# Kernel tuning notes

Hardware: AMD Instinct MI355X
Metric: run time of the kernel (lower is better)

The kernel has to match this reference:

```python
import jax, jax.numpy as jnp
import numpy as np

B, N, D, S = 4, 8, 64, 8192  # batch, heads, dim_head, seq_len


def setup_inputs() -> dict:
    key = jax.random.key(0)
    kq, kk, kv = jax.random.split(key, 3)
    q = jax.random.normal(kq, (B, N, D, S), dtype=jnp.float32)
    k = jax.random.normal(kk, (B, N, D, S), dtype=jnp.float32)
    v = jax.random.normal(kv, (B, N, D, S), dtype=jnp.float32)
    return {"q": q, "k": k, "v": v}


def reference(q, k, v):
    # q, k, v: [b, n, d, s] = [batch, heads, dim_head, seq]
    scale = q.shape[-2] ** -0.5  # dim_head^-0.5
    qs = jax.nn.softmax(q, axis=-2) * scale   # softmax over feature dim
    ks = jax.nn.softmax(k, axis=-1)           # softmax over seq dim
    # kv context: [b, n, d, d] -- avoids the O(s^2) score matrix
    context = jnp.einsum('bnis,bnjs->bnij', ks, v)
    # out: [b, n, d, s]
    return jnp.einsum('bnij,bnis->bnjs', context, qs)
```

## Files before the change

### kernel.cpp

```cpp
#include <hip/hip_runtime.h>
#include <math.h>


typedef _Float16 half8 __attribute__((ext_vector_type(8)));
typedef float floatx4 __attribute__((ext_vector_type(4)));
typedef float floatx16 __attribute__((ext_vector_type(16)));

constexpr int BHEADS = 32;
constexpr int DH     = 64;
constexpr int SEQ    = 8192;
constexpr int NCHUNK = 32;
constexpr float QSCALE = 0.125f;

__device__ __forceinline__ void gload_lds16(const float* g, float* l)
{
    __builtin_amdgcn_global_load_lds(
        (const __attribute__((address_space(1))) void*)g,
        (__attribute__((address_space(3))) void*)l, 16, 0, 0);
}

__global__ __launch_bounds__(256)
void ctx_partial_kernel(const float* __restrict__ K, const float* __restrict__ V,
                        float* __restrict__ partial, float* __restrict__ Zp)
{
    const int head  = blockIdx.y;
    const int chunk = blockIdx.x;
    const int t     = threadIdx.x;
    const int lane  = t & 63;
    const int w     = t >> 6;
    const int ln    = lane & 15;
    const int q8    = lane >> 4;

    const int s0 = chunk * 256;
    const float* kh = K + (size_t)head * DH * SEQ;
    const float* vh = V + (size_t)head * DH * SEQ;

    __shared__ __align__(16) float kbuf[2][64 * 32];
    __shared__ __align__(16) float vbuf[2][64 * 32];

    const int rl = 16 * w + (lane >> 3);
    const int sg = (lane & 7) ^ (rl & 7);
    const float* kg0 = kh + (size_t)rl * SEQ + s0 + sg * 4;
    const float* kg1 = kg0 + (size_t)8 * SEQ;
    const float* vg0 = vh + (size_t)rl * SEQ + s0 + sg * 4;
    const float* vg1 = vg0 + (size_t)8 * SEQ;

#define STAGE(pb, off)                                          \
    do {                                                        \
        gload_lds16(kg0 + (off), &kbuf[pb][(16 * w) * 32]);     \
        gload_lds16(kg1 + (off), &kbuf[pb][(16 * w + 8) * 32]); \
        gload_lds16(vg0 + (off), &vbuf[pb][(16 * w) * 32]);     \
        gload_lds16(vg1 + (off), &vbuf[pb][(16 * w + 8) * 32]); \
    } while (0)

    STAGE(0, 0);
    __syncthreads();

    floatx4 acc[4];
    #pragma unroll
    for (int jt = 0; jt < 4; ++jt) acc[jt] = (floatx4){0.f, 0.f, 0.f, 0.f};
    float zacc = 0.f;

    const int rA = 16 * w + ln;

    #pragma unroll
    for (int step = 0; step < 8; ++step) {
        const int p = step & 1;
        if (step < 7) STAGE(p ^ 1, (step + 1) * 32);
        float e[8];
        #pragma unroll
        for (int eo = 0; eo < 2; ++eo) {
            const int sl = ((q8 * 2 + eo) ^ (rA & 7)) * 4;
            const float4 kv = *(const float4*)(&kbuf[p][rA * 32 + sl]);
            e[eo * 4 + 0] = __expf(kv.x);
            e[eo * 4 + 1] = __expf(kv.y);
            e[eo * 4 + 2] = __expf(kv.z);
            e[eo * 4 + 3] = __expf(kv.w);
        }
        zacc += e[0]+e[1]+e[2]+e[3]+e[4]+e[5]+e[6]+e[7];
        half8 ah;
        #pragma unroll
        for (int x = 0; x < 8; ++x) ah[x] = (_Float16)e[x];
        #pragma unroll
        for (int jt = 0; jt < 4; ++jt) {
            const int rB = 16 * jt + ln;
            half8 bh;
            #pragma unroll
            for (int eo = 0; eo < 2; ++eo) {
                const int sl = ((q8 * 2 + eo) ^ (rB & 7)) * 4;
                const float4 vv = *(const float4*)(&vbuf[p][rB * 32 + sl]);
                bh[eo * 4 + 0] = (_Float16)vv.x;
                bh[eo * 4 + 1] = (_Float16)vv.y;
                bh[eo * 4 + 2] = (_Float16)vv.z;
                bh[eo * 4 + 3] = (_Float16)vv.w;
            }
            acc[jt] = __builtin_amdgcn_mfma_f32_16x16x32_f16(ah, bh, acc[jt], 0, 0, 0);
        }
        if (step < 7) __syncthreads();
    }
#undef STAGE

    float* ph = partial + (size_t)(head * NCHUNK + chunk) * DH * DH;
    #pragma unroll
    for (int jt = 0; jt < 4; ++jt) {
        #pragma unroll
        for (int rr = 0; rr < 4; ++rr) {
            const int i = 16 * w + q8 * 4 + rr;
            const int j = 16 * jt + ln;
            ph[i * DH + j] = acc[jt][rr];
        }
    }

    zacc += __shfl_xor(zacc, 16);
    zacc += __shfl_xor(zacc, 32);
    if (lane < 16)
        Zp[(head * NCHUNK + chunk) * DH + 16 * w + ln] = zacc;
}

__global__ __launch_bounds__(256)
void reduce_kernel(const float* __restrict__ partial, const float* __restrict__ Zp,
                   _Float16* __restrict__ czT)
{
    const int h  = blockIdx.x >> 4;
    const int ig = blockIdx.x & 15;
    const int t  = threadIdx.x;
    const int il = t >> 6;
    const int j  = t & 63;
    const int i  = 4 * ig + il;

    const float* ph = partial + (size_t)h * NCHUNK * DH * DH + i * DH + j;
    float sum = 0.f;
    #pragma unroll
    for (int c = 0; c < NCHUNK; ++c)
        sum += ph[(size_t)c * DH * DH];

    float z = 0.f;
    #pragma unroll
    for (int c = 0; c < NCHUNK; ++c)
        z += Zp[(h * NCHUNK + c) * DH + i];

    czT[(size_t)h * DH * DH + j * DH + i] = (_Float16)(sum / z);
}

__global__ __launch_bounds__(256)
void out_kernel(const float* __restrict__ Q, const _Float16* __restrict__ czT,
                float* __restrict__ out)
{
    const int head = blockIdx.y;
    const int sb   = blockIdx.x;
    const int t    = threadIdx.x;
    const int lane = t & 63;
    const int w    = t >> 6;
    const int l31  = lane & 31;
    const int lh   = lane >> 5;
    const int jw   = 32 * (w & 1);
    const int sw   = 32 * (w >> 1);

    __shared__ __align__(16) float    qf[64 * 68];
    __shared__ __align__(16) _Float16 eqT[64 * 64];
    __shared__ __align__(16) float    wred[64 * 4];

    const float* qh = Q + (size_t)head * DH * SEQ;
    const int r0 = t >> 4;
    const int sc = 4 * (t & 15);
    const int s0 = sb * 128;

    float4 pq[4];
    #pragma unroll
    for (int p = 0; p < 4; ++p)
        pq[p] = *(const float4*)(qh + (size_t)(r0 + 16 * p) * SEQ + s0 + sc);

    const _Float16* ch = czT + (size_t)head * DH * DH;
    half8 afr[4];
    #pragma unroll
    for (int st = 0; st < 4; ++st)
        afr[st] = *(const half8*)(ch + (jw + l31) * DH + st * 16 + lh * 8);

    for (int r = 0; r < 2; ++r) {
        #pragma unroll
        for (int p = 0; p < 4; ++p)
            *(float4*)(qf + (r0 + 16 * p) * 68 + sc) = pq[p];
        if (r < 1) {
            #pragma unroll
            for (int p = 0; p < 4; ++p)
                pq[p] = *(const float4*)(qh + (size_t)(r0 + 16 * p) * SEQ
                                         + s0 + 64 + sc);
        }
        __syncthreads();
        {
            const int s  = t & 63;
            const int cg = t >> 6;
            float wsum = 0.f;
            #pragma unroll
            for (int h2 = 0; h2 < 2; ++h2) {
                const int cc = cg + 4 * h2;
                half8 p8;
                #pragma unroll
                for (int jj = 0; jj < 8; ++jj) {
                    const float e = __expf(qf[(8 * cc + jj) * 68 + s]);
                    wsum += e;
                    p8[jj] = (_Float16)e;
                }
                *(half8*)(eqT + s * 64 + ((cc ^ (s & 7)) * 8)) = p8;
            }
            wred[s * 4 + cg] = wsum;
        }
        __syncthreads();
        const float4 wv = *(const float4*)(wred + (sw + l31) * 4);
        const float rw = QSCALE / (wv.x + wv.y + wv.z + wv.w);
        floatx16 acc = {};
        #pragma unroll
        for (int st = 0; st < 4; ++st) {
            const int s2 = sw + l31;
            const int cc = 2 * st + lh;
            const half8 b = *(const half8*)(eqT + s2 * 64 + ((cc ^ (s2 & 7)) * 8));
            acc = __builtin_amdgcn_mfma_f32_32x32x16_f16(afr[st], b, acc, 0, 0, 0);
        }
        float* oh = out + (size_t)head * DH * SEQ + s0 + r * 64;
        #pragma unroll
        for (int rg = 0; rg < 16; ++rg) {
            const int j = jw + (rg & 3) + 8 * (rg >> 2) + 4 * lh;
            oh[(size_t)j * SEQ + sw + l31] = acc[rg] * rw;
        }
    }
}

extern "C" void kernel_launch(void* const* d_in, const int* in_sizes, int n_in,
                              void* d_out, int out_size, void* d_ws, size_t ws_size,
                              hipStream_t stream)
{
    const float* q = (const float*)d_in[0];
    const float* k = (const float*)d_in[1];
    const float* v = (const float*)d_in[2];
    float* out = (float*)d_out;

    float*    partial = (float*)d_ws;
    float*    Zp      = partial + BHEADS * NCHUNK * DH * DH;
    _Float16* czT     = (_Float16*)(Zp + BHEADS * NCHUNK * DH);

    ctx_partial_kernel<<<dim3(NCHUNK, BHEADS), 256, 0, stream>>>(k, v, partial, Zp);
    reduce_kernel<<<BHEADS * 16, 256, 0, stream>>>(partial, Zp, czT);
    out_kernel<<<dim3(64, BHEADS), 256, 0, stream>>>(q, czT, out);
}
```

Measured before the change: 243.7 us.

## Load Q directly into MFMA B-fragments in out_kernel, dropping LDS staging

The output kernel no longer stages Q through shared memory with a transpose and two barriers. Each lane now reads its Q column values straight from global memory, exponentiates them, and packs them into the MFMA operand. The per-column softmax sum is completed with a cross-lane shuffle. The grid doubles so each block handles 64 sequence positions with one MFMA tile per wave. This removes LDS traffic and synchronization, but the global loads become 32-lane coalesced scalar reads (128B segments) instead of float4 loads, and duplicate Q reads across the two j-halves double the global read volume for Q.

```diff
diff --git a/kernel.cpp b/kernel.cpp
--- a/kernel.cpp
+++ b/kernel.cpp
@@ -154,21 +154,9 @@
     const int l31  = lane & 31;
     const int lh   = lane >> 5;
     const int jw   = 32 * (w & 1);
-    const int sw   = 32 * (w >> 1);
-
-    __shared__ __align__(16) float    qf[64 * 68];
-    __shared__ __align__(16) _Float16 eqT[64 * 64];
-    __shared__ __align__(16) float    wred[64 * 4];
-
-    const float* qh = Q + (size_t)head * DH * SEQ;
-    const int r0 = t >> 4;
-    const int sc = 4 * (t & 15);
-    const int s0 = sb * 128;
-
-    float4 pq[4];
-    #pragma unroll
-    for (int p = 0; p < 4; ++p)
-        pq[p] = *(const float4*)(qh + (size_t)(r0 + 16 * p) * SEQ + s0 + sc);
+    const int s0   = sb * 64 + 32 * (w >> 1);
+
+    const float* qh = Q + (size_t)head * DH * SEQ + s0 + l31;
 
     const _Float16* ch = czT + (size_t)head * DH * DH;
     half8 afr[4];
@@ -176,52 +164,32 @@
     for (int st = 0; st < 4; ++st)
         afr[st] = *(const half8*)(ch + (jw + l31) * DH + st * 16 + lh * 8);
 
-    for (int r = 0; r < 2; ++r) {
-        #pragma unroll
-        for (int p = 0; p < 4; ++p)
-            *(float4*)(qf + (r0 + 16 * p) * 68 + sc) = pq[p];
-        if (r < 1) {
-            #pragma unroll
-            for (int p = 0; p < 4; ++p)
-                pq[p] = *(const float4*)(qh + (size_t)(r0 + 16 * p) * SEQ
-                                         + s0 + 64 + sc);
-        }
-        __syncthreads();
-        {
-            const int s  = t & 63;
-            const int cg = t >> 6;
-            float wsum = 0.f;
-            #pragma unroll
-            for (int h2 = 0; h2 < 2; ++h2) {
-                const int cc = cg + 4 * h2;
-                half8 p8;
-                #pragma unroll
-                for (int jj = 0; jj < 8; ++jj) {
-                    const float e = __expf(qf[(8 * cc + jj) * 68 + s]);
-                    wsum += e;
-                    p8[jj] = (_Float16)e;
-                }
-                *(half8*)(eqT + s * 64 + ((cc ^ (s & 7)) * 8)) = p8;
-            }
-            wred[s * 4 + cg] = wsum;
-        }
-        __syncthreads();
-        const float4 wv = *(const float4*)(wred + (sw + l31) * 4);
-        const float rw = QSCALE / (wv.x + wv.y + wv.z + wv.w);
-        floatx16 acc = {};
-        #pragma unroll
-        for (int st = 0; st < 4; ++st) {
-            const int s2 = sw + l31;
-            const int cc = 2 * st + lh;
-            const half8 b = *(const half8*)(eqT + s2 * 64 + ((cc ^ (s2 & 7)) * 8));
-            acc = __builtin_amdgcn_mfma_f32_32x32x16_f16(afr[st], b, acc, 0, 0, 0);
-        }
-        float* oh = out + (size_t)head * DH * SEQ + s0 + r * 64;
-        #pragma unroll
-        for (int rg = 0; rg < 16; ++rg) {
-            const int j = jw + (rg & 3) + 8 * (rg >> 2) + 4 * lh;
-            oh[(size_t)j * SEQ + sw + l31] = acc[rg] * rw;
-        }
+    floatx16 acc = {};
+    float wsum = 0.f;
+    #pragma unroll
+    for (int st = 0; st < 4; ++st) {
+        float e[8];
+        #pragma unroll
+        for (int kj = 0; kj < 8; ++kj) {
+            const float qv = qh[(size_t)(16 * st + 8 * lh + kj) * SEQ];
+            e[kj] = __expf(qv);
+        }
+        half8 b;
+        #pragma unroll
+        for (int kj = 0; kj < 8; ++kj) {
+            wsum += e[kj];
+            b[kj] = (_Float16)e[kj];
+        }
+        acc = __builtin_amdgcn_mfma_f32_32x32x16_f16(afr[st], b, acc, 0, 0, 0);
+    }
+    wsum += __shfl_xor(wsum, 32);
+    const float rw = QSCALE / wsum;
+
+    float* oh = out + (size_t)head * DH * SEQ + s0 + l31;
+    #pragma unroll
+    for (int rg = 0; rg < 16; ++rg) {
+        const int j = jw + (rg & 3) + 8 * (rg >> 2) + 4 * lh;
+        oh[(size_t)j * SEQ] = acc[rg] * rw;
     }
 }
 
@@ -240,5 +208,5 @@
 
     ctx_partial_kernel<<<dim3(NCHUNK, BHEADS), 256, 0, stream>>>(k, v, partial, Zp);
     reduce_kernel<<<BHEADS * 16, 256, 0, stream>>>(partial, Zp, czT);
-    out_kernel<<<dim3(64, BHEADS), 256, 0, stream>>>(q, czT, out);
-}
+    out_kernel<<<dim3(128, BHEADS), 256, 0, stream>>>(q, czT, out);
+}
```

New measurement: 236.6 us. -2.9%, faster.
